# Kernel optimization log

Hardware: AMD Instinct MI355X
Metric: run time of the kernel (lower is better)

## Reference

```python
import jax, jax.numpy as jnp
import numpy as np

N = 262144      # total line-graph nodes (16 graphs x 16384)
E = 2097152     # total line-graph edges (avg degree 8)
F_IN = 8        # edge_attr feature dim
FEATURES_DIM = 64


def gcn_conv(x, src, dst, W, b, n):
    """PyG GCNConv: x' = D^{-1/2} (A+I) D^{-1/2} (x W) + b, deg from in-edges incl. self-loops."""
    x = x @ W
    loop = jnp.arange(n, dtype=src.dtype)
    si = jnp.concatenate([src, loop])
    di = jnp.concatenate([dst, loop])
    deg = jax.ops.segment_sum(jnp.ones(si.shape[0], dtype=x.dtype), di, num_segments=n)
    dinv = jnp.where(deg > 0, deg ** -0.5, 0.0)
    norm = dinv[si] * dinv[di]                      # [E+N]
    msg = x[si] * norm[:, None]                     # gather + scale
    return jax.ops.segment_sum(msg, di, num_segments=n) + b


def setup_inputs() -> dict:
    key = jax.random.key(0)
    ks = jax.random.split(key, 10)

    def lin(k, fan_in, fan_out):
        return jax.random.normal(k, (fan_in, fan_out), jnp.float32) * (1.0 / np.sqrt(fan_in))

    return {
        "x": jax.random.normal(ks[0], (N, F_IN), jnp.float32),
        "W1": lin(ks[1], F_IN, 16), "b1": jnp.zeros((16,), jnp.float32),
        "W2": lin(ks[2], 16, 32),   "b2": jnp.zeros((32,), jnp.float32),
        "W3": lin(ks[3], 32, 64),   "b3": jnp.zeros((64,), jnp.float32),
        "Wfc": lin(ks[4], 64, FEATURES_DIM), "bfc": jnp.zeros((FEATURES_DIM,), jnp.float32),
        "edge_index": jax.random.randint(ks[5], (2, E), 0, N, dtype=jnp.int32),
        "batch_size": 16,
    }


def reference(x, W1, b1, W2, b2, W3, b3, Wfc, bfc, edge_index, batch_size):
    src, dst = edge_index[0], edge_index[1]
    n = x.shape[0]
    h = jax.nn.relu(gcn_conv(x, src, dst, W1, b1, n))
    h = jax.nn.relu(gcn_conv(h, src, dst, W2, b2, n))
    h = jax.nn.relu(gcn_conv(h, src, dst, W3, b3, n))
    out = h @ Wfc + bfc
    return out.reshape(batch_size, -1, FEATURES_DIM)
```

## Files before the change

kernel.cpp:

```cpp
#include <hip/hip_runtime.h>
#include <hip/hip_bf16.h>


#define NB   256
#define NPB  1024
#define TILE 4096
#define SRCMASK 0x3FFFFu

__device__ __forceinline__ float bf_lo(unsigned u) { return __uint_as_float(u << 16); }
__device__ __forceinline__ float bf_hi(unsigned u) { return __uint_as_float(u & 0xFFFF0000u); }
__device__ __forceinline__ unsigned bf_rne(float f) {
    unsigned b = __float_as_uint(f);
    return (b + 0x7FFFu + ((b >> 16) & 1u)) >> 16;
}

__global__ void hist_kernel(const int* __restrict__ dst, int* __restrict__ ghist,
                            int E, int shift) {
    __shared__ int h[NB];
    int tid = threadIdx.x;
    h[tid] = 0;
    __syncthreads();
    int base = blockIdx.x * TILE;
    int cnt = min(TILE, E - base);
    for (int i = tid; i < cnt; i += 256)
        atomicAdd(&h[dst[base + i] >> shift], 1);
    __syncthreads();
    int v = h[tid];
    if (v) atomicAdd(&ghist[tid], v);
}

__global__ void bscan_kernel(const int* __restrict__ ghist, int* __restrict__ bbase,
                             int* __restrict__ gcursor) {
    __shared__ int sh[NB];
    int tid = threadIdx.x;
    int v = ghist[tid];
    sh[tid] = v;
    __syncthreads();
    for (int o = 1; o < NB; o <<= 1) {
        int t = (tid >= o) ? sh[tid - o] : 0;
        __syncthreads();
        sh[tid] += t;
        __syncthreads();
    }
    int incl = sh[tid];
    bbase[tid] = incl - v;
    gcursor[tid] = incl - v;
    if (tid == NB - 1) bbase[NB] = incl;
}

__global__ void __launch_bounds__(256)
partition_kernel(const int* __restrict__ src, const int* __restrict__ dst,
                 int* __restrict__ gcursor, unsigned int* __restrict__ bedge,
                 int E, int shift, int mask) {
    __shared__ int h[NB], st[NB], gp[NB];
    __shared__ unsigned short rk[TILE];
    __shared__ int sd[TILE];
    __shared__ int ss[TILE];
    int tid = threadIdx.x;
    h[tid] = 0;
    __syncthreads();
    int base = blockIdx.x * TILE;
    int cnt = min(TILE, E - base);
    for (int i = tid; i < cnt; i += 256)
        rk[i] = (unsigned short)atomicAdd(&h[dst[base + i] >> shift], 1);
    __syncthreads();
    int hv = h[tid];
    st[tid] = hv;
    __syncthreads();
    for (int o = 1; o < NB; o <<= 1) {
        int t = (tid >= o) ? st[tid - o] : 0;
        __syncthreads();
        st[tid] += t;
        __syncthreads();
    }
    st[tid] -= hv;
    gp[tid] = hv ? atomicAdd(&gcursor[tid], hv) : 0;
    __syncthreads();
    for (int i = tid; i < cnt; i += 256) {
        int d = dst[base + i];
        int b = d >> shift;
        int pos = st[b] + rk[i];
        sd[pos] = d;
        ss[pos] = src[base + i];
    }
    __syncthreads();
    for (int i = tid; i < cnt; i += 256) {
        int d = sd[i];
        int b = d >> shift;
        int g = gp[b] + (i - st[b]);
        bedge[g] = (unsigned int)ss[i] | ((unsigned int)(d & mask) << 18);
    }
}

__global__ void __launch_bounds__(256)
build_kernel(const int* __restrict__ bbase, const unsigned int* __restrict__ bedge,
             const float* __restrict__ x,
             int* __restrict__ off, float* __restrict__ dinv, int* __restrict__ adj,
             float* __restrict__ y0) {
    __shared__ int deg1[NPB];
    __shared__ int cur[NPB];
    __shared__ int bs[256];
    int tid = threadIdx.x;
    int b = blockIdx.x;
    int s = bbase[b], e = bbase[b + 1];
    int base = tid * 4;
#pragma unroll
    for (int i = 0; i < 4; i++) deg1[base + i] = 0;
    __syncthreads();
    for (int i = s + tid; i < e; i += 256)
        atomicAdd(&deg1[bedge[i] >> 18], 1);
    __syncthreads();
    int d0 = deg1[base], d1 = deg1[base + 1], d2 = deg1[base + 2], d3 = deg1[base + 3];
    int th = d0 + d1 + d2 + d3;
    bs[tid] = th;
    __syncthreads();
    for (int o = 1; o < 256; o <<= 1) {
        int t = (tid >= o) ? bs[tid - o] : 0;
        __syncthreads();
        bs[tid] += t;
        __syncthreads();
    }
    int run = s + bs[tid] - th;
    int vb = b * NPB + base;
    off[vb]     = run; cur[base]     = run; dinv[vb]     = rsqrtf((float)(d0 + 1)); run += d0;
    off[vb + 1] = run; cur[base + 1] = run; dinv[vb + 1] = rsqrtf((float)(d1 + 1)); run += d1;
    off[vb + 2] = run; cur[base + 2] = run; dinv[vb + 2] = rsqrtf((float)(d2 + 1)); run += d2;
    off[vb + 3] = run; cur[base + 3] = run; dinv[vb + 3] = rsqrtf((float)(d3 + 1)); run += d3;
    if (b == NB - 1 && tid == 255) off[NB * NPB] = e;
    __syncthreads();
    for (int i = s + tid; i < e; i += 256) {
        unsigned int pk = bedge[i];
        int p = atomicAdd(&cur[pk >> 18], 1);
        adj[p] = (int)(pk & SRCMASK);
    }
    for (int i = tid; i < NPB * 2; i += 256) {
        int v = i >> 1;
        float dv = rsqrtf((float)(deg1[v] + 1));
        float4 t = ((const float4*)x)[(size_t)b * NPB * 2 + i];
        t.x *= dv; t.y *= dv; t.z *= dv; t.w *= dv;
        ((float4*)y0)[(size_t)b * NPB * 2 + i] = t;
    }
}

__global__ void __launch_bounds__(256)
aggt1_kernel(const float* __restrict__ y0, const int* __restrict__ off,
             const int* __restrict__ adj, const float* __restrict__ dinv,
             const float* __restrict__ W1, const float* __restrict__ b1,
             float* __restrict__ y1) {
    __shared__ float Ws[8 * 16];
    __shared__ float bsh[16];
    __shared__ float sh[128][9];
    const int tid = threadIdx.x;
    if (tid < 128) Ws[tid] = W1[tid];
    if (tid < 16) bsh[tid] = b1[tid];
    const int vbase = blockIdx.x * 128;
    const int vl = tid >> 1, c = tid & 1;
    const int vg = vbase + vl;
    const float4* y4 = (const float4*)y0;
    int beg = off[vg];
    int end = off[vg + 1];
    float4 a0 = y4[(size_t)vg * 2 + c];
    float4 a1, a2, a3;
    a1.x = a1.y = a1.z = a1.w = 0.f;
    a2.x = a2.y = a2.z = a2.w = 0.f;
    a3.x = a3.y = a3.z = a3.w = 0.f;
    int e = beg;
    for (; e + 4 <= end; e += 4) {
        int s0 = adj[e], s1 = adj[e + 1], s2 = adj[e + 2], s3 = adj[e + 3];
        float4 x0 = y4[(size_t)s0 * 2 + c];
        float4 x1 = y4[(size_t)s1 * 2 + c];
        float4 x2 = y4[(size_t)s2 * 2 + c];
        float4 x3 = y4[(size_t)s3 * 2 + c];
        a0.x += x0.x; a0.y += x0.y; a0.z += x0.z; a0.w += x0.w;
        a1.x += x1.x; a1.y += x1.y; a1.z += x1.z; a1.w += x1.w;
        a2.x += x2.x; a2.y += x2.y; a2.z += x2.z; a2.w += x2.w;
        a3.x += x3.x; a3.y += x3.y; a3.z += x3.z; a3.w += x3.w;
    }
    for (; e < end; e++) {
        float4 xs = y4[(size_t)adj[e] * 2 + c];
        a1.x += xs.x; a1.y += xs.y; a1.z += xs.z; a1.w += xs.w;
    }
    float dv = dinv[vg];
    sh[vl][c * 4 + 0] = ((a0.x + a1.x) + (a2.x + a3.x)) * dv;
    sh[vl][c * 4 + 1] = ((a0.y + a1.y) + (a2.y + a3.y)) * dv;
    sh[vl][c * 4 + 2] = ((a0.z + a1.z) + (a2.z + a3.z)) * dv;
    sh[vl][c * 4 + 3] = ((a0.w + a1.w) + (a2.w + a3.w)) * dv;
    __syncthreads();
    const int nl = tid & 127, hf = tid >> 7, j0 = hf * 8;
    float in0 = sh[nl][0], in1 = sh[nl][1], in2 = sh[nl][2], in3 = sh[nl][3];
    float in4 = sh[nl][4], in5 = sh[nl][5], in6 = sh[nl][6], in7 = sh[nl][7];
    float dn = dinv[vbase + nl];
    float o[8];
#pragma unroll
    for (int jj = 0; jj < 8; jj++) {
        int j = j0 + jj;
        float acc = bsh[j];
        acc += in0 * Ws[0 * 16 + j]; acc += in1 * Ws[1 * 16 + j];
        acc += in2 * Ws[2 * 16 + j]; acc += in3 * Ws[3 * 16 + j];
        acc += in4 * Ws[4 * 16 + j]; acc += in5 * Ws[5 * 16 + j];
        acc += in6 * Ws[6 * 16 + j]; acc += in7 * Ws[7 * 16 + j];
        o[jj] = dn * fmaxf(acc, 0.f);
    }
    float4* out4 = (float4*)(y1 + (size_t)(vbase + nl) * 16 + j0);
    float4 t0; t0.x = o[0]; t0.y = o[1]; t0.z = o[2]; t0.w = o[3];
    float4 t1; t1.x = o[4]; t1.y = o[5]; t1.z = o[6]; t1.w = o[7];
    out4[0] = t0; out4[1] = t1;
}

__global__ void __launch_bounds__(256)
aggt2_kernel(const float* __restrict__ y1, const int* __restrict__ off,
             const int* __restrict__ adj, const float* __restrict__ dinv,
             const float* __restrict__ W2, const float* __restrict__ b2,
             unsigned int* __restrict__ y2b) {
    __shared__ float Ws[16 * 32];
    __shared__ float bsh[32];
    __shared__ float sh[64][17];
    const int tid = threadIdx.x;
    for (int i = tid; i < 16 * 32; i += 256) Ws[i] = W2[i];
    if (tid < 32) bsh[tid] = b2[tid];
    const int vbase = blockIdx.x * 64;
    const int vl = tid >> 2, c = tid & 3;
    const int vg = vbase + vl;
    const float4* y4 = (const float4*)y1;
    int beg = off[vg];
    int end = off[vg + 1];
    float4 a0 = y4[(size_t)vg * 4 + c];
    float4 a1, a2, a3;
    a1.x = a1.y = a1.z = a1.w = 0.f;
    a2.x = a2.y = a2.z = a2.w = 0.f;
    a3.x = a3.y = a3.z = a3.w = 0.f;
    int e = beg;
    for (; e + 4 <= end; e += 4) {
        int s0 = adj[e], s1 = adj[e + 1], s2 = adj[e + 2], s3 = adj[e + 3];
        float4 x0 = y4[(size_t)s0 * 4 + c];
        float4 x1 = y4[(size_t)s1 * 4 + c];
        float4 x2 = y4[(size_t)s2 * 4 + c];
        float4 x3 = y4[(size_t)s3 * 4 + c];
        a0.x += x0.x; a0.y += x0.y; a0.z += x0.z; a0.w += x0.w;
        a1.x += x1.x; a1.y += x1.y; a1.z += x1.z; a1.w += x1.w;
        a2.x += x2.x; a2.y += x2.y; a2.z += x2.z; a2.w += x2.w;
        a3.x += x3.x; a3.y += x3.y; a3.z += x3.z; a3.w += x3.w;
    }
    for (; e < end; e++) {
        float4 xs = y4[(size_t)adj[e] * 4 + c];
        a1.x += xs.x; a1.y += xs.y; a1.z += xs.z; a1.w += xs.w;
    }
    float dv = dinv[vg];
    sh[vl][c * 4 + 0] = ((a0.x + a1.x) + (a2.x + a3.x)) * dv;
    sh[vl][c * 4 + 1] = ((a0.y + a1.y) + (a2.y + a3.y)) * dv;
    sh[vl][c * 4 + 2] = ((a0.z + a1.z) + (a2.z + a3.z)) * dv;
    sh[vl][c * 4 + 3] = ((a0.w + a1.w) + (a2.w + a3.w)) * dv;
    __syncthreads();
    const int nl = tid & 63, q = tid >> 6, j0 = q * 8;
    float in[16];
#pragma unroll
    for (int k = 0; k < 16; k++) in[k] = sh[nl][k];
    float dn = dinv[vbase + nl];
    unsigned r[8];
#pragma unroll
    for (int jj = 0; jj < 8; jj++) {
        int j = j0 + jj;
        float acc = bsh[j];
#pragma unroll
        for (int k = 0; k < 16; k++) acc += in[k] * Ws[k * 32 + j];
        r[jj] = bf_rne(dn * fmaxf(acc, 0.f));
    }
    uint4 pk;
    pk.x = r[0] | (r[1] << 16); pk.y = r[2] | (r[3] << 16);
    pk.z = r[4] | (r[5] << 16); pk.w = r[6] | (r[7] << 16);
    ((uint4*)y2b)[(size_t)(vbase + nl) * 4 + q] = pk;
}

__global__ void __launch_bounds__(256)
agg_bf16_kernel(const unsigned int* __restrict__ y2b, const int* __restrict__ off,
                const int* __restrict__ adj, const float* __restrict__ dinv,
                float* __restrict__ a3out, int n) {
    int t = blockIdx.x * 256 + threadIdx.x;
    int v = t >> 2, c = t & 3;
    if (v >= n) return;
    const uint4* yb = (const uint4*)y2b;
    uint4 us = yb[(size_t)v * 4 + c];
    float p0 = bf_lo(us.x), p1 = bf_hi(us.x), p2 = bf_lo(us.y), p3 = bf_hi(us.y);
    float p4 = bf_lo(us.z), p5 = bf_hi(us.z), p6 = bf_lo(us.w), p7 = bf_hi(us.w);
    float q0 = 0, q1 = 0, q2 = 0, q3 = 0, q4 = 0, q5 = 0, q6 = 0, q7 = 0;
    int beg = off[v], end = off[v + 1];
    int e = beg;
    for (; e + 2 <= end; e += 2) {
        int s0 = adj[e], s1 = adj[e + 1];
        uint4 u0 = yb[(size_t)s0 * 4 + c];
        uint4 u1 = yb[(size_t)s1 * 4 + c];
        p0 += bf_lo(u0.x); p1 += bf_hi(u0.x); p2 += bf_lo(u0.y); p3 += bf_hi(u0.y);
        p4 += bf_lo(u0.z); p5 += bf_hi(u0.z); p6 += bf_lo(u0.w); p7 += bf_hi(u0.w);
        q0 += bf_lo(u1.x); q1 += bf_hi(u1.x); q2 += bf_lo(u1.y); q3 += bf_hi(u1.y);
        q4 += bf_lo(u1.z); q5 += bf_hi(u1.z); q6 += bf_lo(u1.w); q7 += bf_hi(u1.w);
    }
    if (e < end) {
        uint4 u0 = yb[(size_t)adj[e] * 4 + c];
        p0 += bf_lo(u0.x); p1 += bf_hi(u0.x); p2 += bf_lo(u0.y); p3 += bf_hi(u0.y);
        p4 += bf_lo(u0.z); p5 += bf_hi(u0.z); p6 += bf_lo(u0.w); p7 += bf_hi(u0.w);
    }
    float dv = dinv[v];
    float4 o0, o1;
    o0.x = (p0 + q0) * dv; o0.y = (p1 + q1) * dv; o0.z = (p2 + q2) * dv; o0.w = (p3 + q3) * dv;
    o1.x = (p4 + q4) * dv; o1.y = (p5 + q5) * dv; o1.z = (p6 + q6) * dv; o1.w = (p7 + q7) * dv;
    float4* out4 = (float4*)a3out;
    out4[(size_t)v * 8 + c * 2]     = o0;
    out4[(size_t)v * 8 + c * 2 + 1] = o1;
}

#define T3_NODES 32
__global__ void __launch_bounds__(256)
t3fc_kernel(const float* __restrict__ in,
            const float* __restrict__ W3, const float* __restrict__ b3,
            const float* __restrict__ Wf, const float* __restrict__ bf,
            float* __restrict__ out, int n) {
    __shared__ float W3s[32 * 64];
    __shared__ float Wfs[64 * 64];
    __shared__ float b3s[64], bfs[64];
    __shared__ float ins[T3_NODES][33];
    __shared__ float tts[T3_NODES][65];
    const int tid = threadIdx.x;
    for (int i = tid; i < 32 * 64; i += 256) W3s[i] = W3[i];
    for (int i = tid; i < 64 * 64; i += 256) Wfs[i] = Wf[i];
    if (tid < 64) { b3s[tid] = b3[tid]; bfs[tid] = bf[tid]; }
    const int vbase = blockIdx.x * T3_NODES;
    {
        const float4* g = (const float4*)(in + (size_t)vbase * 32);
        float4 t = g[tid];
        int v = tid >> 3, c = (tid & 7) * 4;
        ins[v][c] = t.x; ins[v][c + 1] = t.y; ins[v][c + 2] = t.z; ins[v][c + 3] = t.w;
    }
    __syncthreads();
    const int tx = tid & 15;
    const int ty = tid >> 4;
    const int j0 = tx * 4;
    {
        float a00 = b3s[j0], a01 = b3s[j0 + 1], a02 = b3s[j0 + 2], a03 = b3s[j0 + 3];
        float a10 = a00, a11 = a01, a12 = a02, a13 = a03;
#pragma unroll
        for (int k = 0; k < 32; k++) {
            float4 w = *(const float4*)&W3s[k * 64 + j0];
            float x0 = ins[ty][k];
            float x1 = ins[ty + 16][k];
            a00 += x0 * w.x; a01 += x0 * w.y; a02 += x0 * w.z; a03 += x0 * w.w;
            a10 += x1 * w.x; a11 += x1 * w.y; a12 += x1 * w.z; a13 += x1 * w.w;
        }
        tts[ty][j0]          = fmaxf(a00, 0.f); tts[ty][j0 + 1]      = fmaxf(a01, 0.f);
        tts[ty][j0 + 2]      = fmaxf(a02, 0.f); tts[ty][j0 + 3]      = fmaxf(a03, 0.f);
        tts[ty + 16][j0]     = fmaxf(a10, 0.f); tts[ty + 16][j0 + 1] = fmaxf(a11, 0.f);
        tts[ty + 16][j0 + 2] = fmaxf(a12, 0.f); tts[ty + 16][j0 + 3] = fmaxf(a13, 0.f);
    }
    __syncthreads();
    {
        float a00 = bfs[j0], a01 = bfs[j0 + 1], a02 = bfs[j0 + 2], a03 = bfs[j0 + 3];
        float a10 = a00, a11 = a01, a12 = a02, a13 = a03;
#pragma unroll
        for (int k = 0; k < 64; k++) {
            float4 w = *(const float4*)&Wfs[k * 64 + j0];
            float x0 = tts[ty][k];
            float x1 = tts[ty + 16][k];
            a00 += x0 * w.x; a01 += x0 * w.y; a02 += x0 * w.z; a03 += x0 * w.w;
            a10 += x1 * w.x; a11 += x1 * w.y; a12 += x1 * w.z; a13 += x1 * w.w;
        }
        float4 o0; o0.x = a00; o0.y = a01; o0.z = a02; o0.w = a03;
        float4 o1; o1.x = a10; o1.y = a11; o1.z = a12; o1.w = a13;
        *(float4*)(out + ((size_t)(vbase + ty)) * 64 + j0) = o0;
        *(float4*)(out + ((size_t)(vbase + ty + 16)) * 64 + j0) = o1;
    }
}

extern "C" void kernel_launch(void* const* d_in, const int* in_sizes, int n_in,
                              void* d_out, int out_size, void* d_ws, size_t ws_size,
                              hipStream_t stream) {
    const float* x  = (const float*)d_in[0];
    const float* W1 = (const float*)d_in[1];
    const float* b1 = (const float*)d_in[2];
    const float* W2 = (const float*)d_in[3];
    const float* b2 = (const float*)d_in[4];
    const float* W3 = (const float*)d_in[5];
    const float* b3 = (const float*)d_in[6];
    const float* Wf = (const float*)d_in[7];
    const float* bf = (const float*)d_in[8];
    const int*   ei = (const int*)d_in[9];

    const int N = in_sizes[0] / 8;
    const int E = in_sizes[9] / 2;
    const int* srcv = ei;
    const int* dstv = ei + E;
    const int shift = 10;

    char* p = (char*)d_ws;
    auto take = [&p](size_t bytes) { char* q = p; p += (bytes + 63) & ~size_t(63); return q; };
    int*   off   = (int*)take((size_t)(N + 16) * 4);
    float* dinv  = (float*)take((size_t)N * 4);
    int*   adj   = (int*)take((size_t)E * 4);
    int*   ghist = (int*)take(NB * 4);
    int*   bbase = (int*)take((NB + 1) * 4);
    int*   gcur  = (int*)take(NB * 4);
    float* bufA  = (float*)take((size_t)N * 32 * 4);
    float* y1    = (float*)take((size_t)N * 16 * 4);
    char*  regX  = take((size_t)N * 32 * 2);
    unsigned int* bedge = (unsigned int*)regX;
    unsigned int* y2b   = (unsigned int*)regX;
    float* y0 = bufA;

    hipMemsetAsync(ghist, 0, NB * 4, stream);

    int nt = (E + TILE - 1) / TILE;
    hist_kernel<<<nt, 256, 0, stream>>>(dstv, ghist, E, shift);
    bscan_kernel<<<1, NB, 0, stream>>>(ghist, bbase, gcur);
    partition_kernel<<<nt, 256, 0, stream>>>(srcv, dstv, gcur, bedge, E, shift, NPB - 1);
    build_kernel<<<NB, 256, 0, stream>>>(bbase, bedge, x, off, dinv, adj, y0);

    aggt1_kernel<<<N / 128, 256, 0, stream>>>(y0, off, adj, dinv, W1, b1, y1);
    aggt2_kernel<<<N / 64, 256, 0, stream>>>(y1, off, adj, dinv, W2, b2, y2b);
    agg_bf16_kernel<<<(N * 4) / 256, 256, 0, stream>>>(y2b, off, adj, dinv, bufA, N);
    t3fc_kernel<<<N / T3_NODES, 256, 0, stream>>>(bufA, W3, b3, Wf, bf, (float*)d_out, N);
}
```

Before: 345.9 us.

## Compute one node per thread in fused dense layers with weights from global

Restructures the final W3+ReLU+FC kernel so each thread computes one node's full 64-wide output in registers. Weights are read from global memory with wave-uniform addresses instead of being staged in shared memory, and each thread keeps its own row in padded LDS. This drops the per-block weight staging and the block barriers. In exchange it needs 64 accumulators per thread, which raises register pressure and may lower occupancy. Each thread also issues strided 128-byte row loads and 256-byte row stores, which coalesce poorly.

```diff
diff --git a/kernel.cpp b/kernel.cpp
--- a/kernel.cpp
+++ b/kernel.cpp
@@ -308,64 +308,55 @@
     out4[(size_t)v * 8 + c * 2 + 1] = o1;
 }
 
-#define T3_NODES 32
-__global__ void __launch_bounds__(256)
+#define T3_THREADS 128
+#define T3_PITCH   65
+
+__global__ void __launch_bounds__(T3_THREADS)
 t3fc_kernel(const float* __restrict__ in,
             const float* __restrict__ W3, const float* __restrict__ b3,
             const float* __restrict__ Wf, const float* __restrict__ bf,
             float* __restrict__ out, int n) {
-    __shared__ float W3s[32 * 64];
-    __shared__ float Wfs[64 * 64];
-    __shared__ float b3s[64], bfs[64];
-    __shared__ float ins[T3_NODES][33];
-    __shared__ float tts[T3_NODES][65];
+    __shared__ float row[T3_THREADS * T3_PITCH];
     const int tid = threadIdx.x;
-    for (int i = tid; i < 32 * 64; i += 256) W3s[i] = W3[i];
-    for (int i = tid; i < 64 * 64; i += 256) Wfs[i] = Wf[i];
-    if (tid < 64) { b3s[tid] = b3[tid]; bfs[tid] = bf[tid]; }
-    const int vbase = blockIdx.x * T3_NODES;
-    {
-        const float4* g = (const float4*)(in + (size_t)vbase * 32);
-        float4 t = g[tid];
-        int v = tid >> 3, c = (tid & 7) * 4;
-        ins[v][c] = t.x; ins[v][c + 1] = t.y; ins[v][c + 2] = t.z; ins[v][c + 3] = t.w;
-    }
-    __syncthreads();
-    const int tx = tid & 15;
-    const int ty = tid >> 4;
-    const int j0 = tx * 4;
-    {
-        float a00 = b3s[j0], a01 = b3s[j0 + 1], a02 = b3s[j0 + 2], a03 = b3s[j0 + 3];
-        float a10 = a00, a11 = a01, a12 = a02, a13 = a03;
-#pragma unroll
-        for (int k = 0; k < 32; k++) {
-            float4 w = *(const float4*)&W3s[k * 64 + j0];
-            float x0 = ins[ty][k];
-            float x1 = ins[ty + 16][k];
-            a00 += x0 * w.x; a01 += x0 * w.y; a02 += x0 * w.z; a03 += x0 * w.w;
-            a10 += x1 * w.x; a11 += x1 * w.y; a12 += x1 * w.z; a13 += x1 * w.w;
-        }
-        tts[ty][j0]          = fmaxf(a00, 0.f); tts[ty][j0 + 1]      = fmaxf(a01, 0.f);
-        tts[ty][j0 + 2]      = fmaxf(a02, 0.f); tts[ty][j0 + 3]      = fmaxf(a03, 0.f);
-        tts[ty + 16][j0]     = fmaxf(a10, 0.f); tts[ty + 16][j0 + 1] = fmaxf(a11, 0.f);
-        tts[ty + 16][j0 + 2] = fmaxf(a12, 0.f); tts[ty + 16][j0 + 3] = fmaxf(a13, 0.f);
-    }
-    __syncthreads();
-    {
-        float a00 = bfs[j0], a01 = bfs[j0 + 1], a02 = bfs[j0 + 2], a03 = bfs[j0 + 3];
-        float a10 = a00, a11 = a01, a12 = a02, a13 = a03;
-#pragma unroll
-        for (int k = 0; k < 64; k++) {
-            float4 w = *(const float4*)&Wfs[k * 64 + j0];
-            float x0 = tts[ty][k];
-            float x1 = tts[ty + 16][k];
-            a00 += x0 * w.x; a01 += x0 * w.y; a02 += x0 * w.z; a03 += x0 * w.w;
-            a10 += x1 * w.x; a11 += x1 * w.y; a12 += x1 * w.z; a13 += x1 * w.w;
-        }
-        float4 o0; o0.x = a00; o0.y = a01; o0.z = a02; o0.w = a03;
-        float4 o1; o1.x = a10; o1.y = a11; o1.z = a12; o1.w = a13;
-        *(float4*)(out + ((size_t)(vbase + ty)) * 64 + j0) = o0;
-        *(float4*)(out + ((size_t)(vbase + ty + 16)) * 64 + j0) = o1;
+    const int v = blockIdx.x * T3_THREADS + tid;
+    float* my = row + tid * T3_PITCH;
+
+    const float4* g = (const float4*)(in + (size_t)v * 32);
+#pragma unroll
+    for (int c = 0; c < 8; c++) {
+        float4 t = g[c];
+        my[c * 4 + 0] = t.x; my[c * 4 + 1] = t.y;
+        my[c * 4 + 2] = t.z; my[c * 4 + 3] = t.w;
+    }
+
+    float acc[64];
+#pragma unroll
+    for (int j = 0; j < 64; j++) acc[j] = b3[j];
+    for (int k = 0; k < 32; k++) {
+        float xv = my[k];
+        const float* wr = W3 + k * 64;
+#pragma unroll
+        for (int j = 0; j < 64; j++) acc[j] = fmaf(xv, wr[j], acc[j]);
+    }
+#pragma unroll
+    for (int j = 0; j < 64; j++) my[j] = fmaxf(acc[j], 0.f);
+
+#pragma unroll
+    for (int j = 0; j < 64; j++) acc[j] = bf[j];
+    for (int k = 0; k < 64; k++) {
+        float xv = my[k];
+        const float* wr = Wf + k * 64;
+#pragma unroll
+        for (int j = 0; j < 64; j++) acc[j] = fmaf(xv, wr[j], acc[j]);
+    }
+
+    float4* o = (float4*)(out + (size_t)v * 64);
+#pragma unroll
+    for (int c = 0; c < 16; c++) {
+        float4 t;
+        t.x = acc[c * 4 + 0]; t.y = acc[c * 4 + 1];
+        t.z = acc[c * 4 + 2]; t.w = acc[c * 4 + 3];
+        o[c] = t;
     }
 }
 
@@ -415,5 +406,5 @@
     aggt1_kernel<<<N / 128, 256, 0, stream>>>(y0, off, adj, dinv, W1, b1, y1);
     aggt2_kernel<<<N / 64, 256, 0, stream>>>(y1, off, adj, dinv, W2, b2, y2b);
     agg_bf16_kernel<<<(N * 4) / 256, 256, 0, stream>>>(y2b, off, adj, dinv, bufA, N);
-    t3fc_kernel<<<N / T3_NODES, 256, 0, stream>>>(bufA, W3, b3, Wf, bf, (float*)d_out, N);
-}
+    t3fc_kernel<<<N / T3_THREADS, T3_THREADS, 0, stream>>>(bufA, W3, b3, Wf, bf, (float*)d_out, N);
+}
```

After: 381.7 us. 10.3% more time.
